# Performance work log

Hardware: AMD Instinct MI355X
Metric: run time of the kernel (lower is better)

## Reference

```python
import jax, jax.numpy as jnp
import numpy as np

N = 100000   # nodes
E = 1600000  # edges
D = 128      # input_dim
H = 128      # hidden_dim
CH = 16      # cluster_hidden_dim
P = 10       # processor_nodes


def setup_inputs() -> dict:
    key = jax.random.key(0)
    ks = jax.random.split(key, 22)
    s = 0.05
    return {
        "x": jax.random.normal(ks[0], (N, D), jnp.float32),
        "edges": jax.random.randint(ks[1], (2, E), 0, N, dtype=jnp.int32),
        "edge_attr": jax.random.uniform(ks[2], (E,), jnp.float32),
        "ready": jax.random.randint(ks[3], (N, 1), 0, 2, dtype=jnp.int32),
        "proc_emb": jax.random.normal(ks[4], (P, 3), jnp.float32),
        # GCN layers (PyG GCNConv: lin without bias, explicit bias added after aggregation)
        "gcn_w": jax.random.normal(ks[5], (2, D, H), jnp.float32) * s,
        "gcn_b": jax.random.normal(ks[6], (2, H), jnp.float32) * s,
        # listmlp: Linear(H,H) -> relu, then Linear(H,1)
        "mlp_w1": jax.random.normal(ks[7], (H, H), jnp.float32) * s,
        "mlp_b1": jax.random.normal(ks[8], (H,), jnp.float32) * s,
        "mlp_w2": jax.random.normal(ks[9], (H, 1), jnp.float32) * s,
        "mlp_b2": jax.random.normal(ks[10], (1,), jnp.float32) * s,
        # listmlp_value: Linear(H,1)
        "val_w": jax.random.normal(ks[11], (H, 1), jnp.float32) * s,
        "val_b": jax.random.normal(ks[12], (1,), jnp.float32) * s,
        # cluster_linear: Linear(3*P, CH)
        "cl_w": jax.random.normal(ks[13], (3 * P, CH), jnp.float32) * s,
        "cl_b": jax.random.normal(ks[14], (CH,), jnp.float32) * s,
        # listmlp_pass: Linear(H+CH,H) -> relu, then Linear(H,1)
        "pass_w1": jax.random.normal(ks[15], (H + CH, H), jnp.float32) * s,
        "pass_b1": jax.random.normal(ks[16], (H,), jnp.float32) * s,
        "pass_w2": jax.random.normal(ks[17], (H, 1), jnp.float32) * s,
        "pass_b2": jax.random.normal(ks[18], (1,), jnp.float32) * s,
    }


def _gcn_layer(x, row, col, w_e, W, b):
    # PyG GCNConv with flow='target_to_source': out[row] += norm_e * (x @ W)[col]
    # gcn_norm with idx=row: deg[i] = sum of edge weights with row==i (self-loops included)
    h = x @ W                                              # [N,H]
    deg = jax.ops.segment_sum(w_e, row, num_segments=N)    # [N]
    dis = jnp.where(deg > 0, jax.lax.rsqrt(deg), 0.0)      # deg^-1/2, inf -> 0
    norm = dis[row] * w_e * dis[col]                       # [E+N]
    msg = h[col] * norm[:, None]                           # [E+N,H] gather
    out = jax.ops.segment_sum(msg, row, num_segments=N)    # [N,H] scatter-add
    return out + b


def _forward(x, edges, edge_attr, ready, proc_emb, gcn_w, gcn_b,
             mlp_w1, mlp_b1, mlp_w2, mlp_b2, val_w, val_b, cl_w, cl_b,
             pass_w1, pass_b1, pass_w2, pass_b2):
    # add self-loops with weight 1 (GCNConv default add_self_loops=True)
    loop = jnp.arange(N, dtype=edges.dtype)
    row = jnp.concatenate([edges[0], loop])
    col = jnp.concatenate([edges[1], loop])
    w_e = jnp.concatenate([edge_attr, jnp.ones((N,), edge_attr.dtype)])

    h = x
    for l in range(2):
        h = jax.nn.relu(_gcn_layer(h, row, col, w_e, gcn_w[l], gcn_b[l]))

    mask = ready[:, 0] > 0                                 # [N] bool
    v = jnp.mean(h, axis=0)                                # [H]
    x_pass = jnp.max(jnp.where(mask[:, None], h, -jnp.inf), axis=0)  # masked max, [H]

    fc = proc_emb.reshape(-1) @ cl_w + cl_b                # [CH]
    x_pass = jnp.concatenate([x_pass, fc], axis=0)         # [H+CH]

    v = v @ val_w + val_b                                  # [1]

    logits = jax.nn.relu(h @ mlp_w1 + mlp_b1) @ mlp_w2 + mlp_b2        # [N,1]
    x_pass = jax.nn.relu(x_pass @ pass_w1 + pass_b1) @ pass_w2 + pass_b2  # [1]

    # torch indexes logits[ready]; here we mask non-ready entries with -inf so
    # the softmax over [N+1] matches torch's values on the ready rows.
    node_logits = jnp.where(mask, logits[:, 0], -jnp.inf)
    probs = jax.nn.softmax(jnp.concatenate([node_logits, x_pass], axis=0))  # [N+1]
    return probs, v


def reference(x, edges, edge_attr, ready, proc_emb, gcn_w, gcn_b,
              mlp_w1, mlp_b1, mlp_w2, mlp_b2, val_w, val_b, cl_w, cl_b,
              pass_w1, pass_b1, pass_w2, pass_b2):
    return _forward(x, edges, edge_attr, ready, proc_emb, gcn_w, gcn_b,
                    mlp_w1, mlp_b1, mlp_w2, mlp_b2, val_w, val_b, cl_w, cl_b,
                    pass_w1, pass_b1, pass_w2, pass_b2)
```

## Files before the change

### kernel.cpp

```cpp
#include <hip/hip_runtime.h>
#include <cstdint>

#define NN 100000
#define EE 1600000
#define HH 128
#define NREP 8
#define PSZ (NN / 8)
#define HPP (PSZ / 2)
#define SS 64
#define CAP 300000
#define NBB 500
#define BCH 3200
#define SCAN_CHUNK 512
#define NSCAN ((NN + SCAN_CHUNK - 1) / SCAN_CHUNK)

typedef unsigned long long u64;
typedef unsigned short ushort;
typedef unsigned char uchar;
typedef __attribute__((ext_vector_type(8))) short bf16x8;
typedef __attribute__((ext_vector_type(4))) float f32x4;
typedef __attribute__((ext_vector_type(2))) float f32x2;

__device__ __forceinline__ ushort f2bf(float x) {
    union { float f; unsigned u; } v; v.f = x;
    unsigned r = v.u + 0x7fffu + ((v.u >> 16) & 1u);
    return (ushort)(r >> 16);
}
__device__ __forceinline__ float bf2f(unsigned h16) {
    union { unsigned u; float f; } v; v.u = h16 << 16; return v.f;
}

__device__ __forceinline__ uchar f2fp8(float a) {
    return (uchar)(__builtin_amdgcn_cvt_pk_fp8_f32(a, a, 0, false) & 0xff);
}
__device__ __forceinline__ void unpack8_fp8(uint2 q, float* v) {
    f32x2 a = __builtin_amdgcn_cvt_pk_f32_fp8(q.x, false);
    f32x2 b = __builtin_amdgcn_cvt_pk_f32_fp8(q.x, true);
    f32x2 c = __builtin_amdgcn_cvt_pk_f32_fp8(q.y, false);
    f32x2 d = __builtin_amdgcn_cvt_pk_f32_fp8(q.y, true);
    v[0] = a[0]; v[1] = a[1]; v[2] = b[0]; v[3] = b[1];
    v[4] = c[0]; v[5] = c[1]; v[6] = d[0]; v[7] = d[1];
}

__device__ __forceinline__ unsigned encf(float f) {
    int b = __float_as_int(f);
    return (b >= 0) ? ((unsigned)b | 0x80000000u) : ~(unsigned)b;
}
__device__ __forceinline__ float decf(unsigned u) {
    return (u & 0x80000000u) ? __int_as_float((int)(u & 0x7fffffffu))
                             : __int_as_float((int)(~u));
}
#define ENC_NEG_INF 0x007FFFFFu

__global__ void k_setup(float* __restrict__ meansum, unsigned* __restrict__ maxenc,
                        unsigned* __restrict__ lmaxenc, float* __restrict__ esum,
                        int* __restrict__ gtail,
                        const float* __restrict__ w0, const float* __restrict__ w1,
                        const float* __restrict__ w2, ushort* __restrict__ wt) {
    int idx = blockIdx.x * blockDim.x + threadIdx.x;
    if (idx < NREP * HH) { meansum[idx] = 0.f; maxenc[idx] = ENC_NEG_INF; }
    if (idx < 8) gtail[idx] = 0;
    if (idx == 0) { lmaxenc[0] = ENC_NEG_INF; esum[0] = 0.f; }
    if (idx < 3 * HH * HH) {
        int mat = idx >> 14;
        int e = idx & 16383;
        int n = e >> 7, k = e & 127;
        const float* src = (mat == 0) ? w0 : (mat == 1) ? w1 : w2;
        wt[idx] = f2bf(src[k * HH + n]);
    }
}

__global__ __launch_bounds__(256) void k_bucket(const int* __restrict__ rows,
                                                const int* __restrict__ cols,
                                                const float* __restrict__ ea,
                                                int* __restrict__ gtail,
                                                u64* __restrict__ ebuck) {
    __shared__ u64 buf[8][1024];
    __shared__ int cnt8[8];
    __shared__ int rsv[8];
    int t = threadIdx.x;
    if (t < 8) cnt8[t] = 0;
    __syncthreads();
    int e0 = blockIdx.x * BCH;
    int e1 = e0 + BCH;
    for (int ebase = e0; ebase < e1; ebase += 1024) {
        int e = ebase + t * 4;
        if (e < e1) {
            int4 r4 = *(const int4*)(rows + e);
            int4 c4 = *(const int4*)(cols + e);
            float4 a4 = *(const float4*)(ea + e);
            int rr[4] = {r4.x, r4.y, r4.z, r4.w};
            int cc[4] = {c4.x, c4.y, c4.z, c4.w};
            float aa[4] = {a4.x, a4.y, a4.z, a4.w};
#pragma unroll
            for (int j = 0; j < 4; ++j) {
                int p = rr[j] / PSZ;
                int rl = rr[j] - p * PSZ;
                unsigned q = (unsigned)(aa[j] * 32767.0f + 0.5f);
                u64 en = ((u64)rl << 32) | (u64)(((unsigned)cc[j] << 15) | q);
                int idx = atomicAdd(&cnt8[p], 1);
                buf[p][idx] = en;
            }
        }
        __syncthreads();
        if (t < 8) rsv[t] = atomicAdd(&gtail[t], cnt8[t]);
        __syncthreads();
#pragma unroll
        for (int p = 0; p < 8; ++p) {
            int nn = cnt8[p], oo = rsv[p];
            u64* dst = ebuck + (size_t)p * CAP + oo;
            for (int j = t; j < nn; j += 256) dst[j] = buf[p][j];
        }
        __syncthreads();
        if (t < 8) cnt8[t] = 0;
        __syncthreads();
    }
}

__global__ __launch_bounds__(256) void k_cnt2(const u64* __restrict__ ebuck,
                                              const int* __restrict__ gtail,
                                              unsigned* __restrict__ cntp) {
    __shared__ unsigned h32[HPP];
    int b = blockIdx.x;
    int s = b >> 3, p = b & 7;
    for (int j = threadIdx.x; j < HPP; j += 256) h32[j] = 0;
    __syncthreads();
    int pc = gtail[p];
    int len = (pc + SS - 1) / SS;
    int lo = s * len, hi = min(lo + len, pc);
    const u64* src = ebuck + (size_t)p * CAP;
    for (int i = lo + threadIdx.x; i < hi; i += 256) {
        int rl = (int)(src[i] >> 32);
        atomicAdd(&h32[rl >> 1], (rl & 1) ? 0x10000u : 1u);
    }
    __syncthreads();
    unsigned* dst = cntp + (size_t)(p * SS + s) * HPP;
    for (int j = threadIdx.x; j < HPP; j += 256) dst[j] = h32[j];
}

__global__ void k_rowdelta(const unsigned* __restrict__ cntp, int* __restrict__ count,
                           unsigned* __restrict__ deltap) {
    int rp = blockIdx.x * blockDim.x + threadIdx.x;
    if (rp >= NN / 2) return;
    int p = rp / HPP, j = rp - p * HPP;
    unsigned s0 = 0, s1 = 0;
#pragma unroll 8
    for (int c = 0; c < SS; ++c) {
        size_t o = (size_t)(p * SS + c) * HPP + j;
        unsigned v = cntp[o];
        deltap[o] = s0 | (s1 << 16);
        s0 += v & 0xffffu;
        s1 += v >> 16;
    }
    int r0 = p * PSZ + 2 * j;
    *(int2*)(count + r0) = make_int2((int)s0, (int)s1);
}

__global__ void k_scan1(const int* __restrict__ cnt, int* __restrict__ out,
                        int* __restrict__ bsum) {
    int b = blockIdx.x, t = threadIdx.x;
    int i0 = b * SCAN_CHUNK + t * 2;
    int c0 = (i0 < NN) ? cnt[i0] : 0;
    int c1 = (i0 + 1 < NN) ? cnt[i0 + 1] : 0;
    c0 = (c0 + 7) & ~7;
    c1 = (c1 + 7) & ~7;
    int s = c0 + c1;
    int lane = t & 63, w = t >> 6;
    int v = s;
#pragma unroll
    for (int off = 1; off < 64; off <<= 1) {
        int u = __shfl_up(v, off, 64);
        if (lane >= off) v += u;
    }
    __shared__ int wsum[4];
    if (lane == 63) wsum[w] = v;
    __syncthreads();
    int wadd = 0;
    for (int j = 0; j < w; ++j) wadd += wsum[j];
    int incl = v + wadd;
    int excl = incl - s;
    if (i0 < NN) out[i0] = excl;
    if (i0 + 1 < NN) out[i0 + 1] = excl + c0;
    if (t == 255) bsum[b] = incl;
}

__global__ void k_scan2(int* __restrict__ bsum, int* __restrict__ base) {
    __shared__ int tmp[256];
    int t = threadIdx.x;
    int v = (t < NSCAN) ? bsum[t] : 0;
    tmp[t] = v;
    __syncthreads();
    for (int off = 1; off < 256; off <<= 1) {
        int u = (t >= off) ? tmp[t - off] : 0;
        __syncthreads();
        tmp[t] += u;
        __syncthreads();
    }
    if (t == NSCAN - 1) base[NN] = tmp[t];
    if (t < NSCAN) bsum[t] = tmp[t] - v;
}

__global__ void k_scan3(int* __restrict__ out, const int* __restrict__ bsum) {
    int i = blockIdx.x * blockDim.x + threadIdx.x;
    if (i < NN) out[i] += bsum[i / SCAN_CHUNK];
}

__global__ __launch_bounds__(256) void k_fill2(const u64* __restrict__ ebuck,
                                               const int* __restrict__ gtail,
                                               const unsigned* __restrict__ deltap,
                                               const int* __restrict__ base,
                                               unsigned* __restrict__ csre) {
    __shared__ int nxt[PSZ];
    int b = blockIdx.x;
    int s = b >> 3, p = b & 7;
    const unsigned* dsrc = deltap + (size_t)(p * SS + s) * HPP;
    const int* bsrc = base + p * PSZ;
    for (int j = threadIdx.x; j < HPP; j += 256) {
        unsigned d = dsrc[j];
        int2 bb = *(const int2*)(bsrc + 2 * j);
        nxt[2 * j] = bb.x + (int)(d & 0xffffu);
        nxt[2 * j + 1] = bb.y + (int)(d >> 16);
    }
    __syncthreads();
    int pc = gtail[p];
    int len = (pc + SS - 1) / SS;
    int lo = s * len, hi = min(lo + len, pc);
    const u64* src = ebuck + (size_t)p * CAP;
    for (int i = lo + threadIdx.x; i < hi; i += 256) {
        u64 en = src[i];
        int rl = (int)(en >> 32);
        int slot = atomicAdd(&nxt[rl], 1);
        csre[slot] = (unsigned)(en & 0xffffffffu);
    }
}

__global__ void k_degsum(const int* __restrict__ count, unsigned* __restrict__ csre,
                         const int* __restrict__ base, float* __restrict__ dis) {
    int r = blockIdx.x * blockDim.x + threadIdx.x;
    if (r >= NN) return;
    int lo = base[r], hip = base[r + 1];
    int hireal = lo + count[r];
    float s = 0.f;
    for (int e = lo; e < hireal; ++e) s += (float)(csre[e] & 0x7fffu);
    unsigned selfv = (unsigned)r << 15;
    for (int e = hireal; e < hip; ++e) csre[e] = selfv;
    dis[r] = rsqrtf(1.0f + s * (1.0f / 32767.0f));
}

__global__ __launch_bounds__(256) void k_gather(const uchar* __restrict__ hW,
                                                const unsigned* __restrict__ csre,
                                                const int* __restrict__ base,
                                                const float* __restrict__ dis,
                                                const float* __restrict__ bias,
                                                ushort* __restrict__ agg) {
    int node = blockIdx.x * 16 + (threadIdx.x >> 4);
    if (node >= NN) return;
    int l = threadIdx.x & 15;
    int f = l * 8;
    int lo = base[node], hi = base[node + 1];
    float disn = dis[node];
    float wk = disn * (1.0f / 32767.0f);
    float acc[8];
    {
        uint2 q = *(const uint2*)(hW + (size_t)node * HH + f);
        float v[8]; unpack8_fp8(q, v);
#pragma unroll
        for (int j = 0; j < 8; ++j) acc[j] = disn * v[j];
    }
    for (int eb = lo; eb < hi; eb += 8) {
        uint4 pa = *(const uint4*)(csre + eb);
        uint4 pb = *(const uint4*)(csre + eb + 4);
        unsigned pp[8] = {pa.x, pa.y, pa.z, pa.w, pb.x, pb.y, pb.z, pb.w};
        uint2 qq[8];
#pragma unroll
        for (int j = 0; j < 8; ++j)
            qq[j] = *(const uint2*)(hW + (size_t)(pp[j] >> 15) * HH + f);
#pragma unroll
        for (int j = 0; j < 8; ++j) {
            float w = (float)(pp[j] & 0x7fffu) * wk;
            float v[8]; unpack8_fp8(qq[j], v);
#pragma unroll
            for (int k = 0; k < 8; ++k) acc[k] += w * v[k];
        }
    }
    float4 b0 = *(const float4*)(bias + f);
    float4 b1 = *(const float4*)(bias + f + 4);
    ushort o[8];
    o[0] = f2bf(acc[0] + b0.x); o[1] = f2bf(acc[1] + b0.y);
    o[2] = f2bf(acc[2] + b0.z); o[3] = f2bf(acc[3] + b0.w);
    o[4] = f2bf(acc[4] + b1.x); o[5] = f2bf(acc[5] + b1.y);
    o[6] = f2bf(acc[6] + b1.z); o[7] = f2bf(acc[7] + b1.w);
    *(uint4*)(agg + (size_t)node * HH + f) = *(uint4*)o;
}

template <int MODE>
__global__ __launch_bounds__(256) void k_mfma(const void* __restrict__ Ain,
                                              const ushort* __restrict__ Wt,
                                              uchar* __restrict__ C,
                                              const float* __restrict__ dis,
                                              const float* __restrict__ b1,
                                              const float* __restrict__ w2v,
                                              const float* __restrict__ b2,
                                              const int* __restrict__ ready,
                                              float* __restrict__ logits,
                                              float* __restrict__ meansum,
                                              unsigned* __restrict__ maxenc,
                                              unsigned* __restrict__ lmaxenc, int n) {
    __shared__ ushort As[64 * HH];
    __shared__ ushort Ws[128 * HH];
    __shared__ int rdy[64];
    __shared__ unsigned slmax;
    const int t = threadIdx.x;
    const int rb = blockIdx.x * 64;
    if (MODE == 2) {
        if (t < 64) rdy[t] = (rb + t < n) ? ready[rb + t] : 0;
        if (t == 0) slmax = ENC_NEG_INF;
    }
#pragma unroll
    for (int i = 0; i < 8; ++i) {
        int nr = i * 16 + (t >> 4);
        int gc = t & 15;
        uint4 q = *(const uint4*)(Wt + (size_t)nr * HH + gc * 8);
        *(uint4*)(Ws + nr * HH + ((gc ^ (nr & 15)) * 8)) = q;
    }
#pragma unroll
    for (int i = 0; i < 4; ++i) {
        int m = i * 16 + (t >> 4);
        int k = (t & 15) * 8;
        ushort pk[8];
        if (MODE == 0) {
            const float* Af = (const float*)Ain;
            float4 v0 = make_float4(0.f, 0.f, 0.f, 0.f), v1 = v0;
            if (rb + m < n) {
                const float* src = Af + (size_t)(rb + m) * HH + k;
                v0 = *(const float4*)src;
                v1 = *(const float4*)(src + 4);
            }
            pk[0] = f2bf(v0.x); pk[1] = f2bf(v0.y); pk[2] = f2bf(v0.z); pk[3] = f2bf(v0.w);
            pk[4] = f2bf(v1.x); pk[5] = f2bf(v1.y); pk[6] = f2bf(v1.z); pk[7] = f2bf(v1.w);
        } else {
            const ushort* Au = (const ushort*)Ain;
            uint4 q = make_uint4(0, 0, 0, 0);
            if (rb + m < n) q = *(const uint4*)(Au + (size_t)(rb + m) * HH + k);
            *(uint4*)pk = q;
#pragma unroll
            for (int j = 0; j < 8; ++j) pk[j] = (pk[j] & 0x8000) ? (ushort)0 : pk[j];
        }
        int gsw = (t & 15) ^ (m & 15);
        *(uint4*)(As + m * HH + gsw * 8) = *(uint4*)pk;
    }
    __syncthreads();

    const int wave = t >> 6, lane = t & 63;
    const int cl = lane & 15;
    const int kq = lane >> 4;
    const int m0 = wave * 16;

    f32x4 acc[8];
#pragma unroll
    for (int c = 0; c < 8; ++c) acc[c] = (f32x4){0.f, 0.f, 0.f, 0.f};

#pragma unroll
    for (int kk = 0; kk < 4; ++kk) {
        int g = kk * 4 + kq;
        bf16x8 bfr = *(const bf16x8*)(As + (m0 + cl) * HH + ((g ^ cl) * 8));
#pragma unroll
        for (int c = 0; c < 8; ++c) {
            bf16x8 afr = *(const bf16x8*)(Ws + (c * 16 + cl) * HH + ((g ^ cl) * 8));
            acc[c] = __builtin_amdgcn_mfma_f32_16x16x32_bf16(afr, bfr, acc[c], 0, 0, 0);
        }
    }

    const int node = rb + m0 + cl;
    if (MODE < 2) {
        if (node < n) {
            float d = dis[node];
            uchar* dst = C + (size_t)node * HH + kq * 4;
#pragma unroll
            for (int c = 0; c < 8; ++c) {
                unsigned u = __builtin_amdgcn_cvt_pk_fp8_f32(acc[c][0] * d, acc[c][1] * d, 0u, false);
                u = __builtin_amdgcn_cvt_pk_fp8_f32(acc[c][2] * d, acc[c][3] * d, u, true);
                *(unsigned*)(dst + c * 16) = u;
            }
        }
    } else {
        float s = 0.f;
#pragma unroll
        for (int c = 0; c < 8; ++c) {
            float4 bb = *(const float4*)(b1 + c * 16 + kq * 4);
            float4 ww = *(const float4*)(w2v + c * 16 + kq * 4);
            s += fmaxf(acc[c][0] + bb.x, 0.f) * ww.x;
            s += fmaxf(acc[c][1] + bb.y, 0.f) * ww.y;
            s += fmaxf(acc[c][2] + bb.z, 0.f) * ww.z;
            s += fmaxf(acc[c][3] + bb.w, 0.f) * ww.w;
        }
        s += __shfl_xor(s, 16, 64);
        s += __shfl_xor(s, 32, 64);
        unsigned mylmax = ENC_NEG_INF;
        if (kq == 0 && node < n) {
            float lg = s + b2[0];
            logits[node] = lg;
            if (rdy[m0 + cl] > 0) mylmax = encf(lg);
        }
        if (mylmax != ENC_NEG_INF) atomicMax(&slmax, mylmax);

        int lim = min(64, n - rb);
        if (t < HH) {
            int f = t, gf = f >> 3, fo = f & 7;
            float sum = 0.f, mx = -3.4e38f;
            for (int m = 0; m < lim; ++m) {
                float v = bf2f(As[m * HH + ((gf ^ (m & 15)) * 8) + fo]);
                sum += v;
                if (rdy[m] > 0) mx = fmaxf(mx, v);
            }
            int rep = blockIdx.x & (NREP - 1);
            atomicAdd(&meansum[rep * HH + f], sum);
            if (mx > -3.0e38f) atomicMax(&maxenc[rep * HH + f], encf(mx));
        }
        __syncthreads();
        if (t == 0 && slmax != ENC_NEG_INF) atomicMax(lmaxenc, slmax);
    }
}

__global__ void k_fin1(const float* __restrict__ meansum, const unsigned* __restrict__ maxenc,
                       const unsigned* __restrict__ lmaxenc,
                       const float* __restrict__ val_w, const float* __restrict__ val_b,
                       const float* __restrict__ pe, const float* __restrict__ cl_w,
                       const float* __restrict__ cl_b, const float* __restrict__ pw1,
                       const float* __restrict__ pb1, const float* __restrict__ pw2,
                       const float* __restrict__ pb2, float* __restrict__ scal,
                       float* __restrict__ d_out) {
    __shared__ float xp[144];
    __shared__ float msum[HH];
    __shared__ float zp[HH];
    int t = threadIdx.x;
    if (t < HH) {
        float s = 0.f;
        unsigned mx = ENC_NEG_INF;
#pragma unroll
        for (int r = 0; r < NREP; ++r) {
            s += meansum[r * HH + t];
            unsigned e = maxenc[r * HH + t];
            if (e > mx) mx = e;
        }
        msum[t] = s;
        xp[t] = decf(mx);
    } else if (t < 144) {
        int c = t - HH;
        float s = cl_b[c];
        for (int k = 0; k < 30; ++k) s += pe[k] * cl_w[k * 16 + c];
        xp[t] = s;
    }
    __syncthreads();
    if (t < HH) {
        float s = pb1[t];
        for (int k = 0; k < 144; ++k) s += xp[k] * pw1[k * HH + t];
        zp[t] = fmaxf(s, 0.f);
    }
    __syncthreads();
    if (t < 64) {
        float s1 = zp[t] * pw2[t] + zp[t + 64] * pw2[t + 64];
        float s2 = msum[t] * val_w[t] + msum[t + 64] * val_w[t + 64];
#pragma unroll
        for (int off = 32; off > 0; off >>= 1) {
            s1 += __shfl_xor(s1, off, 64);
            s2 += __shfl_xor(s2, off, 64);
        }
        if (t == 0) {
            float xpass = s1 + pb2[0];
            float v = s2 * (1.0f / NN) + val_b[0];
            float M = fmaxf(decf(lmaxenc[0]), xpass);
            scal[0] = M;
            scal[1] = expf(xpass - M);
            d_out[NN + 1] = v;
        }
    }
}

__global__ __launch_bounds__(256) void k_exp(const float* __restrict__ logits,
                                             const int* __restrict__ ready,
                                             const float* __restrict__ scal,
                                             float* __restrict__ d_out,
                                             float* __restrict__ esum) {
    __shared__ float warr[4];
    int t = threadIdx.x;
    int i = blockIdx.x * 256 + t;
    float M = scal[0];
    float p = 0.f;
    if (i < NN) {
        if (ready[i] > 0) p = expf(logits[i] - M);
        d_out[i] = p;
    }
    float s = p;
#pragma unroll
    for (int off = 32; off > 0; off >>= 1) s += __shfl_xor(s, off, 64);
    if ((t & 63) == 0) warr[t >> 6] = s;
    __syncthreads();
    if (t == 0) atomicAdd(esum, warr[0] + warr[1] + warr[2] + warr[3]);
}

__global__ void k_scale(const float* __restrict__ esum, const float* __restrict__ scal,
                        float* __restrict__ d_out) {
    int i = blockIdx.x * blockDim.x + threadIdx.x;
    float inv = 1.0f / (esum[0] + scal[1]);
    if (i < NN) d_out[i] *= inv;
    else if (i == NN) d_out[NN] = scal[1] * inv;
}

extern "C" void kernel_launch(void* const* d_in, const int* in_sizes, int n_in,
                              void* d_out, int out_size, void* d_ws, size_t ws_size,
                              hipStream_t stream) {
    const float* x      = (const float*)d_in[0];
    const int*   edges  = (const int*)d_in[1];
    const float* eattr  = (const float*)d_in[2];
    const int*   ready  = (const int*)d_in[3];
    const float* pe     = (const float*)d_in[4];
    const float* gcn_w  = (const float*)d_in[5];
    const float* gcn_b  = (const float*)d_in[6];
    const float* mlp_w1 = (const float*)d_in[7];
    const float* mlp_b1 = (const float*)d_in[8];
    const float* mlp_w2 = (const float*)d_in[9];
    const float* mlp_b2 = (const float*)d_in[10];
    const float* val_w  = (const float*)d_in[11];
    const float* val_b  = (const float*)d_in[12];
    const float* cl_w   = (const float*)d_in[13];
    const float* cl_b   = (const float*)d_in[14];
    const float* pw1    = (const float*)d_in[15];
    const float* pb1    = (const float*)d_in[16];
    const float* pw2    = (const float*)d_in[17];
    const float* pb2    = (const float*)d_in[18];

    const int* rows = edges;
    const int* cols = edges + EE;

    char* P = (char*)d_ws;
    size_t off = 0;
    auto carve = [&](size_t bytes) {
        off = (off + 255) & ~(size_t)255;
        void* p = P + off;
        off += bytes;
        return p;
    };
    float* dis     = (float*)carve(NN * 4);
    float* logits  = (float*)carve(NN * 4);
    int*   count   = (int*)carve(NN * 4);
    int*   base    = (int*)carve((NN + 1) * 4);
    int*   bsum    = (int*)carve(256 * 4);
    ushort* bufB   = (ushort*)carve((size_t)NN * HH * 2);
    uchar* bufH    = (uchar*)carve((size_t)NN * HH);
    unsigned* csre = (unsigned*)carve((size_t)(EE + 8 * NN) * 4);
    u64*   ebuck   = (u64*)carve((size_t)8 * CAP * 8);
    float* meansum = (float*)carve(NREP * HH * 4);
    unsigned* maxenc = (unsigned*)carve(NREP * HH * 4);
    unsigned* lmaxenc = (unsigned*)carve(4);
    float* esum    = (float*)carve(4);
    float* scal    = (float*)carve(8);
    int*   gtail   = (int*)carve(8 * 4);
    ushort* wt     = (ushort*)carve(3 * HH * HH * 2);

    unsigned* cntp   = (unsigned*)bufB;
    unsigned* deltap = (unsigned*)bufB + (size_t)8 * SS * HPP;

    float* out = (float*)d_out;

    const int nb = (NN + 255) / 256;
    const int gb = (NN + 63) / 64;
    const int ab = (NN + 15) / 16;
    const int pb = 8 * SS;

    k_setup<<<(3 * HH * HH + 255) / 256, 256, 0, stream>>>(meansum, maxenc, lmaxenc, esum,
                                                           gtail, gcn_w, gcn_w + HH * HH,
                                                           mlp_w1, wt);

    k_bucket<<<NBB, 256, 0, stream>>>(rows, cols, eattr, gtail, ebuck);
    k_cnt2<<<pb, 256, 0, stream>>>(ebuck, gtail, cntp);
    k_rowdelta<<<(NN / 2 + 255) / 256, 256, 0, stream>>>(cntp, count, deltap);
    k_scan1<<<NSCAN, 256, 0, stream>>>(count, base, bsum);
    k_scan2<<<1, 256, 0, stream>>>(bsum, base);
    k_scan3<<<nb, 256, 0, stream>>>(base, bsum);
    k_fill2<<<pb, 256, 0, stream>>>(ebuck, gtail, deltap, base, csre);
    k_degsum<<<nb, 256, 0, stream>>>(count, csre, base, dis);

    k_mfma<0><<<gb, 256, 0, stream>>>(x, wt, bufH, dis, nullptr, nullptr, nullptr, nullptr,
                                      nullptr, nullptr, nullptr, nullptr, NN);
    k_gather<<<ab, 256, 0, stream>>>(bufH, csre, base, dis, gcn_b, bufB);

    k_mfma<1><<<gb, 256, 0, stream>>>(bufB, wt + HH * HH, bufH, dis, nullptr, nullptr, nullptr,
                                      nullptr, nullptr, nullptr, nullptr, nullptr, NN);
    k_gather<<<ab, 256, 0, stream>>>(bufH, csre, base, dis, gcn_b + HH, bufB);

    k_mfma<2><<<gb, 256, 0, stream>>>(bufB, wt + 2 * HH * HH, nullptr, nullptr, mlp_b1, mlp_w2,
                                      mlp_b2, ready, logits, meansum, maxenc, lmaxenc, NN);
    k_fin1<<<1, 256, 0, stream>>>(meansum, maxenc, lmaxenc, val_w, val_b, pe, cl_w, cl_b,
                                  pw1, pb1, pw2, pb2, scal, out);
    k_exp<<<nb, 256, 0, stream>>>(logits, ready, scal, out, esum);
    k_scale<<<(NN + 1 + 255) / 256, 256, 0, stream>>>(esum, scal, out);
}
```

Before: 339.0 us.

## Widen GEMM row tile to 128 and unroll aggregation gathers by 16

```diff
diff --git a/kernel.cpp b/kernel.cpp
--- a/kernel.cpp
+++ b/kernel.cpp
@@ -162,8 +162,8 @@
     int i0 = b * SCAN_CHUNK + t * 2;
     int c0 = (i0 < NN) ? cnt[i0] : 0;
     int c1 = (i0 + 1 < NN) ? cnt[i0 + 1] : 0;
-    c0 = (c0 + 7) & ~7;
-    c1 = (c1 + 7) & ~7;
+    c0 = (c0 + 15) & ~15;
+    c1 = (c1 + 15) & ~15;
     int s = c0 + c1;
     int lane = t & 63, w = t >> 6;
     int v = s;
@@ -267,16 +267,19 @@
 #pragma unroll
         for (int j = 0; j < 8; ++j) acc[j] = disn * v[j];
     }
-    for (int eb = lo; eb < hi; eb += 8) {
+    for (int eb = lo; eb < hi; eb += 16) {
         uint4 pa = *(const uint4*)(csre + eb);
         uint4 pb = *(const uint4*)(csre + eb + 4);
-        unsigned pp[8] = {pa.x, pa.y, pa.z, pa.w, pb.x, pb.y, pb.z, pb.w};
-        uint2 qq[8];
-#pragma unroll
-        for (int j = 0; j < 8; ++j)
+        uint4 pc = *(const uint4*)(csre + eb + 8);
+        uint4 pd = *(const uint4*)(csre + eb + 12);
+        unsigned pp[16] = {pa.x, pa.y, pa.z, pa.w, pb.x, pb.y, pb.z, pb.w,
+                           pc.x, pc.y, pc.z, pc.w, pd.x, pd.y, pd.z, pd.w};
+        uint2 qq[16];
+#pragma unroll
+        for (int j = 0; j < 16; ++j)
             qq[j] = *(const uint2*)(hW + (size_t)(pp[j] >> 15) * HH + f);
 #pragma unroll
-        for (int j = 0; j < 8; ++j) {
+        for (int j = 0; j < 16; ++j) {
             float w = (float)(pp[j] & 0x7fffu) * wk;
             float v[8]; unpack8_fp8(qq[j], v);
 #pragma unroll
@@ -306,14 +309,14 @@
                                               float* __restrict__ meansum,
                                               unsigned* __restrict__ maxenc,
                                               unsigned* __restrict__ lmaxenc, int n) {
-    __shared__ ushort As[64 * HH];
+    __shared__ ushort As[128 * HH];
     __shared__ ushort Ws[128 * HH];
-    __shared__ int rdy[64];
+    __shared__ int rdy[128];
     __shared__ unsigned slmax;
     const int t = threadIdx.x;
-    const int rb = blockIdx.x * 64;
+    const int rb = blockIdx.x * 128;
     if (MODE == 2) {
-        if (t < 64) rdy[t] = (rb + t < n) ? ready[rb + t] : 0;
+        if (t < 128) rdy[t] = (rb + t < n) ? ready[rb + t] : 0;
         if (t == 0) slmax = ENC_NEG_INF;
     }
 #pragma unroll
@@ -324,7 +327,7 @@
         *(uint4*)(Ws + nr * HH + ((gc ^ (nr & 15)) * 8)) = q;
     }
 #pragma unroll
-    for (int i = 0; i < 4; ++i) {
+    for (int i = 0; i < 8; ++i) {
         int m = i * 16 + (t >> 4);
         int k = (t & 15) * 8;
         ushort pk[8];
@@ -354,57 +357,89 @@
     const int wave = t >> 6, lane = t & 63;
     const int cl = lane & 15;
     const int kq = lane >> 4;
-    const int m0 = wave * 16;
-
-    f32x4 acc[8];
-#pragma unroll
-    for (int c = 0; c < 8; ++c) acc[c] = (f32x4){0.f, 0.f, 0.f, 0.f};
+    const int r0 = wave * 32 + cl;
+    const int r1 = r0 + 16;
+
+    f32x4 acc0[8], acc1[8];
+#pragma unroll
+    for (int c = 0; c < 8; ++c) {
+        acc0[c] = (f32x4){0.f, 0.f, 0.f, 0.f};
+        acc1[c] = (f32x4){0.f, 0.f, 0.f, 0.f};
+    }
 
 #pragma unroll
     for (int kk = 0; kk < 4; ++kk) {
         int g = kk * 4 + kq;
-        bf16x8 bfr = *(const bf16x8*)(As + (m0 + cl) * HH + ((g ^ cl) * 8));
+        int so = (g ^ cl) * 8;
+        bf16x8 a0 = *(const bf16x8*)(As + r0 * HH + so);
+        bf16x8 a1 = *(const bf16x8*)(As + r1 * HH + so);
 #pragma unroll
         for (int c = 0; c < 8; ++c) {
-            bf16x8 afr = *(const bf16x8*)(Ws + (c * 16 + cl) * HH + ((g ^ cl) * 8));
-            acc[c] = __builtin_amdgcn_mfma_f32_16x16x32_bf16(afr, bfr, acc[c], 0, 0, 0);
-        }
-    }
-
-    const int node = rb + m0 + cl;
+            bf16x8 b = *(const bf16x8*)(Ws + (c * 16 + cl) * HH + so);
+            acc0[c] = __builtin_amdgcn_mfma_f32_16x16x32_bf16(b, a0, acc0[c], 0, 0, 0);
+            acc1[c] = __builtin_amdgcn_mfma_f32_16x16x32_bf16(b, a1, acc1[c], 0, 0, 0);
+        }
+    }
+
+    const int node0 = rb + r0;
+    const int node1 = node0 + 16;
     if (MODE < 2) {
-        if (node < n) {
-            float d = dis[node];
-            uchar* dst = C + (size_t)node * HH + kq * 4;
+        if (node0 < n) {
+            float d = dis[node0];
+            uchar* dst = C + (size_t)node0 * HH + kq * 4;
 #pragma unroll
             for (int c = 0; c < 8; ++c) {
-                unsigned u = __builtin_amdgcn_cvt_pk_fp8_f32(acc[c][0] * d, acc[c][1] * d, 0u, false);
-                u = __builtin_amdgcn_cvt_pk_fp8_f32(acc[c][2] * d, acc[c][3] * d, u, true);
+                unsigned u = __builtin_amdgcn_cvt_pk_fp8_f32(acc0[c][0] * d, acc0[c][1] * d, 0u, false);
+                u = __builtin_amdgcn_cvt_pk_fp8_f32(acc0[c][2] * d, acc0[c][3] * d, u, true);
                 *(unsigned*)(dst + c * 16) = u;
             }
         }
+        if (node1 < n) {
+            float d = dis[node1];
+            uchar* dst = C + (size_t)node1 * HH + kq * 4;
+#pragma unroll
+            for (int c = 0; c < 8; ++c) {
+                unsigned u = __builtin_amdgcn_cvt_pk_fp8_f32(acc1[c][0] * d, acc1[c][1] * d, 0u, false);
+                u = __builtin_amdgcn_cvt_pk_fp8_f32(acc1[c][2] * d, acc1[c][3] * d, u, true);
+                *(unsigned*)(dst + c * 16) = u;
+            }
+        }
     } else {
-        float s = 0.f;
+        float s0 = 0.f, s1 = 0.f;
 #pragma unroll
         for (int c = 0; c < 8; ++c) {
             float4 bb = *(const float4*)(b1 + c * 16 + kq * 4);
             float4 ww = *(const float4*)(w2v + c * 16 + kq * 4);
-            s += fmaxf(acc[c][0] + bb.x, 0.f) * ww.x;
-            s += fmaxf(acc[c][1] + bb.y, 0.f) * ww.y;
-            s += fmaxf(acc[c][2] + bb.z, 0.f) * ww.z;
-            s += fmaxf(acc[c][3] + bb.w, 0.f) * ww.w;
-        }
-        s += __shfl_xor(s, 16, 64);
-        s += __shfl_xor(s, 32, 64);
+            s0 += fmaxf(acc0[c][0] + bb.x, 0.f) * ww.x;
+            s0 += fmaxf(acc0[c][1] + bb.y, 0.f) * ww.y;
+            s0 += fmaxf(acc0[c][2] + bb.z, 0.f) * ww.z;
+            s0 += fmaxf(acc0[c][3] + bb.w, 0.f) * ww.w;
+            s1 += fmaxf(acc1[c][0] + bb.x, 0.f) * ww.x;
+            s1 += fmaxf(acc1[c][1] + bb.y, 0.f) * ww.y;
+            s1 += fmaxf(acc1[c][2] + bb.z, 0.f) * ww.z;
+            s1 += fmaxf(acc1[c][3] + bb.w, 0.f) * ww.w;
+        }
+        s0 += __shfl_xor(s0, 16, 64);
+        s0 += __shfl_xor(s0, 32, 64);
+        s1 += __shfl_xor(s1, 16, 64);
+        s1 += __shfl_xor(s1, 32, 64);
         unsigned mylmax = ENC_NEG_INF;
-        if (kq == 0 && node < n) {
-            float lg = s + b2[0];
-            logits[node] = lg;
-            if (rdy[m0 + cl] > 0) mylmax = encf(lg);
+        if (kq == 0) {
+            float b2s = b2[0];
+            if (node0 < n) {
+                float lg = s0 + b2s;
+                logits[node0] = lg;
+                if (rdy[r0] > 0) { unsigned e = encf(lg); if (e > mylmax) mylmax = e; }
+            }
+            if (node1 < n) {
+                float lg = s1 + b2s;
+                logits[node1] = lg;
+                if (rdy[r1] > 0) { unsigned e = encf(lg); if (e > mylmax) mylmax = e; }
+            }
         }
         if (mylmax != ENC_NEG_INF) atomicMax(&slmax, mylmax);
 
-        int lim = min(64, n - rb);
+        int lim = min(128, n - rb);
         if (t < HH) {
             int f = t, gf = f >> 3, fo = f & 7;
             float sum = 0.f, mx = -3.4e38f;
@@ -548,7 +583,7 @@
     int*   bsum    = (int*)carve(256 * 4);
     ushort* bufB   = (ushort*)carve((size_t)NN * HH * 2);
     uchar* bufH    = (uchar*)carve((size_t)NN * HH);
-    unsigned* csre = (unsigned*)carve((size_t)(EE + 8 * NN) * 4);
+    unsigned* csre = (unsigned*)carve((size_t)(EE + 16 * NN) * 4);
     u64*   ebuck   = (u64*)carve((size_t)8 * CAP * 8);
     float* meansum = (float*)carve(NREP * HH * 4);
     unsigned* maxenc = (unsigned*)carve(NREP * HH * 4);
@@ -564,7 +599,7 @@
     float* out = (float*)d_out;
 
     const int nb = (NN + 255) / 256;
-    const int gb = (NN + 63) / 64;
+    const int gb = (NN + 127) / 128;
     const int ab = (NN + 15) / 16;
     const int pb = 8 * SS;
 
```

Measured after the change: 349.3 us. 3.0% more time.

## Fuse row-delta with block scan and fold scan fixup into consumers

Applied to the files above, without the earlier changes.

```diff
diff --git a/kernel.cpp b/kernel.cpp
--- a/kernel.cpp
+++ b/kernel.cpp
@@ -138,30 +138,26 @@
     for (int j = threadIdx.x; j < HPP; j += 256) dst[j] = h32[j];
 }
 
-__global__ void k_rowdelta(const unsigned* __restrict__ cntp, int* __restrict__ count,
-                           unsigned* __restrict__ deltap) {
-    int rp = blockIdx.x * blockDim.x + threadIdx.x;
-    if (rp >= NN / 2) return;
-    int p = rp / HPP, j = rp - p * HPP;
-    unsigned s0 = 0, s1 = 0;
+__global__ void k_cntscan(const unsigned* __restrict__ cntp, int* __restrict__ count,
+                          unsigned* __restrict__ deltap, int* __restrict__ basep,
+                          int* __restrict__ bsum) {
+    int b = blockIdx.x, t = threadIdx.x;
+    int rp = b * 256 + t;
+    int c0 = 0, c1 = 0;
+    if (rp < NN / 2) {
+        int p = rp / HPP, j = rp - p * HPP;
+        unsigned s0 = 0, s1 = 0;
 #pragma unroll 8
-    for (int c = 0; c < SS; ++c) {
-        size_t o = (size_t)(p * SS + c) * HPP + j;
-        unsigned v = cntp[o];
-        deltap[o] = s0 | (s1 << 16);
-        s0 += v & 0xffffu;
-        s1 += v >> 16;
-    }
-    int r0 = p * PSZ + 2 * j;
-    *(int2*)(count + r0) = make_int2((int)s0, (int)s1);
-}
-
-__global__ void k_scan1(const int* __restrict__ cnt, int* __restrict__ out,
-                        int* __restrict__ bsum) {
-    int b = blockIdx.x, t = threadIdx.x;
-    int i0 = b * SCAN_CHUNK + t * 2;
-    int c0 = (i0 < NN) ? cnt[i0] : 0;
-    int c1 = (i0 + 1 < NN) ? cnt[i0 + 1] : 0;
+        for (int c = 0; c < SS; ++c) {
+            size_t o = (size_t)(p * SS + c) * HPP + j;
+            unsigned v = cntp[o];
+            deltap[o] = s0 | (s1 << 16);
+            s0 += v & 0xffffu;
+            s1 += v >> 16;
+        }
+        c0 = (int)s0; c1 = (int)s1;
+        *(int2*)(count + 2 * rp) = make_int2(c0, c1);
+    }
     c0 = (c0 + 7) & ~7;
     c1 = (c1 + 7) & ~7;
     int s = c0 + c1;
@@ -179,8 +175,9 @@
     for (int j = 0; j < w; ++j) wadd += wsum[j];
     int incl = v + wadd;
     int excl = incl - s;
-    if (i0 < NN) out[i0] = excl;
-    if (i0 + 1 < NN) out[i0 + 1] = excl + c0;
+    int i0 = 2 * rp;
+    if (i0 < NN) basep[i0] = excl;
+    if (i0 + 1 < NN) basep[i0 + 1] = excl + c0;
     if (t == 255) bsum[b] = incl;
 }
 
@@ -200,26 +197,23 @@
     if (t < NSCAN) bsum[t] = tmp[t] - v;
 }
 
-__global__ void k_scan3(int* __restrict__ out, const int* __restrict__ bsum) {
-    int i = blockIdx.x * blockDim.x + threadIdx.x;
-    if (i < NN) out[i] += bsum[i / SCAN_CHUNK];
-}
-
 __global__ __launch_bounds__(256) void k_fill2(const u64* __restrict__ ebuck,
                                                const int* __restrict__ gtail,
                                                const unsigned* __restrict__ deltap,
-                                               const int* __restrict__ base,
+                                               const int* __restrict__ basep,
+                                               const int* __restrict__ bsum,
                                                unsigned* __restrict__ csre) {
     __shared__ int nxt[PSZ];
     int b = blockIdx.x;
     int s = b >> 3, p = b & 7;
     const unsigned* dsrc = deltap + (size_t)(p * SS + s) * HPP;
-    const int* bsrc = base + p * PSZ;
+    const int* bsrc = basep + p * PSZ;
     for (int j = threadIdx.x; j < HPP; j += 256) {
         unsigned d = dsrc[j];
         int2 bb = *(const int2*)(bsrc + 2 * j);
-        nxt[2 * j] = bb.x + (int)(d & 0xffffu);
-        nxt[2 * j + 1] = bb.y + (int)(d >> 16);
+        int badd = bsum[(p * PSZ + 2 * j) >> 9];
+        nxt[2 * j] = bb.x + badd + (int)(d & 0xffffu);
+        nxt[2 * j + 1] = bb.y + badd + (int)(d >> 16);
     }
     __syncthreads();
     int pc = gtail[p];
@@ -235,10 +229,13 @@
 }
 
 __global__ void k_degsum(const int* __restrict__ count, unsigned* __restrict__ csre,
-                         const int* __restrict__ base, float* __restrict__ dis) {
+                         const int* __restrict__ basep, const int* __restrict__ bsum,
+                         int* __restrict__ base, float* __restrict__ dis) {
     int r = blockIdx.x * blockDim.x + threadIdx.x;
     if (r >= NN) return;
-    int lo = base[r], hip = base[r + 1];
+    int lo = basep[r] + bsum[r >> 9];
+    int hip = (r == NN - 1) ? base[NN] : (basep[r + 1] + bsum[(r + 1) >> 9]);
+    base[r] = lo;
     int hireal = lo + count[r];
     float s = 0.f;
     for (int e = lo; e < hireal; ++e) s += (float)(csre[e] & 0x7fffu);
@@ -544,6 +541,7 @@
     float* dis     = (float*)carve(NN * 4);
     float* logits  = (float*)carve(NN * 4);
     int*   count   = (int*)carve(NN * 4);
+    int*   basep   = (int*)carve(NN * 4);
     int*   base    = (int*)carve((NN + 1) * 4);
     int*   bsum    = (int*)carve(256 * 4);
     ushort* bufB   = (ushort*)carve((size_t)NN * HH * 2);
@@ -574,12 +572,10 @@
 
     k_bucket<<<NBB, 256, 0, stream>>>(rows, cols, eattr, gtail, ebuck);
     k_cnt2<<<pb, 256, 0, stream>>>(ebuck, gtail, cntp);
-    k_rowdelta<<<(NN / 2 + 255) / 256, 256, 0, stream>>>(cntp, count, deltap);
-    k_scan1<<<NSCAN, 256, 0, stream>>>(count, base, bsum);
+    k_cntscan<<<NSCAN, 256, 0, stream>>>(cntp, count, deltap, basep, bsum);
     k_scan2<<<1, 256, 0, stream>>>(bsum, base);
-    k_scan3<<<nb, 256, 0, stream>>>(base, bsum);
-    k_fill2<<<pb, 256, 0, stream>>>(ebuck, gtail, deltap, base, csre);
-    k_degsum<<<nb, 256, 0, stream>>>(count, csre, base, dis);
+    k_fill2<<<pb, 256, 0, stream>>>(ebuck, gtail, deltap, basep, bsum, csre);
+    k_degsum<<<nb, 256, 0, stream>>>(count, csre, basep, bsum, base, dis);
 
     k_mfma<0><<<gb, 256, 0, stream>>>(x, wt, bufH, dis, nullptr, nullptr, nullptr, nullptr,
                                       nullptr, nullptr, nullptr, nullptr, NN);
```

New measurement: 341.2 us. Within noise of the previous version (+0.7%).
